# Kernel tuning notes

Hardware: AMD Instinct MI355X
Metric: run time of the kernel (lower is better)

## Reference

```python
import jax, jax.numpy as jnp
import numpy as np

N_NODES = 100000
N_EDGES = 1600000
D_FEAT = 128
HIDDEN = 128
HEADS = 4
OUT_C = HIDDEN // HEADS  # 32
N_CLASSES = 10
N_GRAPHS = 64
NEG_SLOPE = 0.2


def glorot(key, shape, fan_in, fan_out):
    s = jnp.sqrt(6.0 / (fan_in + fan_out))
    return jax.random.uniform(key, shape, minval=-s, maxval=s, dtype=jnp.float32)


def setup_inputs() -> dict:
    key = jax.random.key(0)
    ks = jax.random.split(key, 24)
    x = jax.random.normal(ks[0], (N_NODES, D_FEAT), dtype=jnp.float32)
    src = jax.random.randint(ks[1], (N_EDGES,), 0, N_NODES, dtype=jnp.int32)
    off = jax.random.randint(ks[2], (N_EDGES,), 1, N_NODES, dtype=jnp.int32)
    dst = ((src + off) % N_NODES).astype(jnp.int32)  # guarantees no self-loops
    edge_index = jnp.stack([src, dst], axis=0)
    batch = jnp.sort(jax.random.randint(ks[3], (N_NODES,), 0, N_GRAPHS, dtype=jnp.int32))
    inp = {"x": x, "edge_index": edge_index, "batch": batch}
    # GATConv layer params: W [in, H*C] (lin_l == lin_r), att_l/att_r [H, C], bias [H*C]
    ins = [D_FEAT, HIDDEN, HIDDEN]
    for i in range(3):
        k = 4 + 4 * i
        inp[f"W{i+1}"] = glorot(ks[k], (ins[i], HEADS * OUT_C), ins[i], HEADS * OUT_C)
        inp[f"al{i+1}"] = glorot(ks[k + 1], (HEADS, OUT_C), HEADS * OUT_C, 1)
        inp[f"ar{i+1}"] = glorot(ks[k + 2], (HEADS, OUT_C), HEADS * OUT_C, 1)
        inp[f"b{i+1}"] = jnp.zeros((HEADS * OUT_C,), jnp.float32)
    inp["lin1_w"] = glorot(ks[16], (HIDDEN, HIDDEN), HIDDEN, HIDDEN)
    inp["lin1_b"] = jnp.zeros((HIDDEN,), jnp.float32)
    inp["lin2_w"] = glorot(ks[17], (HIDDEN, N_CLASSES), HIDDEN, N_CLASSES)
    inp["lin2_b"] = jnp.zeros((N_CLASSES,), jnp.float32)
    return inp


def gat_layer(x, src, dst, W, att_l, att_r, bias):
    n = x.shape[0]
    H, C = att_l.shape
    xw = (x @ W).reshape(n, H, C)                       # Theta x
    al = jnp.einsum('nhc,hc->nh', xw, att_l)
    ar = jnp.einsum('nhc,hc->nh', xw, att_r)
    loop = jnp.arange(n, dtype=src.dtype)
    s = jnp.concatenate([src, loop])                    # add self-loops
    d = jnp.concatenate([dst, loop])
    logits = jax.nn.leaky_relu(al[s] + ar[d], NEG_SLOPE)  # [E+N, H]
    m = jax.ops.segment_max(logits, d, num_segments=n)    # segment softmax over dst
    e = jnp.exp(logits - m[d])
    z = jax.ops.segment_sum(e, d, num_segments=n)
    alpha = e / z[d]
    msg = xw[s] * alpha[:, :, None]                     # [E+N, H, C]
    out = jax.ops.segment_sum(msg, d, num_segments=n)   # scatter-add aggregate
    return out.reshape(n, H * C) + bias


def reference(x, edge_index, batch,
              W1, al1, ar1, b1, W2, al2, ar2, b2, W3, al3, ar3, b3,
              lin1_w, lin1_b, lin2_w, lin2_b):
    src, dst = edge_index[0], edge_index[1]
    h = jax.nn.relu(gat_layer(x, src, dst, W1, al1, ar1, b1))
    h = jax.nn.relu(gat_layer(h, src, dst, W2, al2, ar2, b2))
    h = jax.nn.relu(gat_layer(h, src, dst, W3, al3, ar3, b3))
    last = h
    # global mean pool over graphs in the batch
    s = jax.ops.segment_sum(h, batch, num_segments=N_GRAPHS)
    cnt = jax.ops.segment_sum(jnp.ones((h.shape[0],), h.dtype), batch, num_segments=N_GRAPHS)
    pooled = s / jnp.maximum(cnt, 1.0)[:, None]
    g = jax.nn.relu(pooled @ lin1_w + lin1_b)           # dropout inactive (eval)
    logits = g @ lin2_w + lin2_b
    return (jax.nn.log_softmax(logits, axis=-1), last)
```

## Files before the change

kernel.cpp:

```cpp
#include <hip/hip_runtime.h>
#include <math.h>


#define LRELU(x) ((x) > 0.f ? (x) : 0.2f*(x))
#define SH 8
#define TILE 4096
#define EPT 16
#define PSL 64

typedef __attribute__((ext_vector_type(8))) short s16x8;
typedef __attribute__((ext_vector_type(4))) float f32x4;

__device__ inline unsigned short f2bf(float f){
  unsigned u = __float_as_uint(f);
  u += 0x7fff + ((u >> 16) & 1);
  return (unsigned short)(u >> 16);
}

__global__ void k_init(int* __restrict__ bcnt, float* __restrict__ psum){
  int t = threadIdx.x;
  bcnt[t] = 0; bcnt[256 + t] = 0;
  for (int i = t; i < 8192; i += 256) psum[i] = 0.f;
}

template<bool BF16IN>
__device__ __forceinline__ void gemm_body(
    unsigned short* Wt, unsigned short* Xl,
    const void* __restrict__ Xv, const float* __restrict__ W,
    const float* __restrict__ attl, const float* __restrict__ attr,
    unsigned short* __restrict__ XW, float* __restrict__ AL, float* __restrict__ AR,
    int n, int bid, int gstride)
{
  int t = threadIdx.x;
  int lane = t & 63, w = t >> 6;
  int l15 = lane & 15, quad = lane >> 4;
  for (int i = 0; i < 64; i++){
    int e = i*256 + t;
    int k = e >> 7, nn = e & 127;
    Wt[nn*128 + ((((k>>3) ^ (nn&15))<<3) | (k&7))] = f2bf(W[e]);
  }
  int ntiles = (n + 63) >> 6;
  int r_ = t >> 2, seg = t & 3;
  for (int tile = bid; tile < ntiles; tile += gstride){
    int row0 = tile << 6;
    __syncthreads();
    {
      int grow = row0 + r_;
      unsigned short* dp = &Xl[r_*136 + seg*32];
      if (grow < n){
        if (BF16IN){
          const uint4* gp = (const uint4*)((const unsigned short*)Xv + (size_t)grow*128 + seg*32);
          #pragma unroll
          for (int i = 0; i < 4; i++) ((uint4*)dp)[i] = gp[i];
        } else {
          const float4* gp = (const float4*)((const float*)Xv + (size_t)grow*128 + seg*32);
          #pragma unroll
          for (int i = 0; i < 8; i++){
            float4 v = gp[i];
            ((unsigned*)dp)[i*2]   = (unsigned)f2bf(v.x) | ((unsigned)f2bf(v.y) << 16);
            ((unsigned*)dp)[i*2+1] = (unsigned)f2bf(v.z) | ((unsigned)f2bf(v.w) << 16);
          }
        }
      } else {
        #pragma unroll
        for (int i = 0; i < 4; i++) ((uint4*)dp)[i] = make_uint4(0,0,0,0);
      }
    }
    __syncthreads();
    f32x4 acc[4][2];
    #pragma unroll
    for (int rt = 0; rt < 4; rt++){ acc[rt][0] = (f32x4){0,0,0,0}; acc[rt][1] = (f32x4){0,0,0,0}; }
    #pragma unroll
    for (int ks = 0; ks < 4; ks++){
      s16x8 b0 = *(const s16x8*)&Wt[(w*32 + l15)*128      + (((ks*4+quad) ^ l15)<<3)];
      s16x8 b1 = *(const s16x8*)&Wt[(w*32 + 16 + l15)*128 + (((ks*4+quad) ^ l15)<<3)];
      #pragma unroll
      for (int rt = 0; rt < 4; rt++){
        s16x8 a = *(const s16x8*)&Xl[(rt*16 + l15)*136 + ks*32 + quad*8];
        acc[rt][0] = __builtin_amdgcn_mfma_f32_16x16x32_bf16(a, b0, acc[rt][0], 0, 0, 0);
        acc[rt][1] = __builtin_amdgcn_mfma_f32_16x16x32_bf16(a, b1, acc[rt][1], 0, 0, 0);
      }
    }
    __syncthreads();
    #pragma unroll
    for (int rt = 0; rt < 4; rt++)
      #pragma unroll
      for (int c2 = 0; c2 < 2; c2++)
        #pragma unroll
        for (int r = 0; r < 4; r++)
          Xl[(rt*16 + quad*4 + r)*136 + w*32 + c2*16 + l15] = f2bf(acc[rt][c2][r]);
    __syncthreads();
    {
      int grow = row0 + r_;
      if (grow < n){
        const unsigned short* sp = &Xl[r_*136 + seg*32];
        uint4 uu[4];
        #pragma unroll
        for (int i = 0; i < 4; i++) uu[i] = ((const uint4*)sp)[i];
        unsigned short* gx = XW + (size_t)grow*128 + seg*32;
        #pragma unroll
        for (int i = 0; i < 4; i++) ((uint4*)gx)[i] = uu[i];
        const unsigned* up = (const unsigned*)uu;
        const float4* alp = (const float4*)(attl + seg*32);
        const float4* arp = (const float4*)(attr + seg*32);
        float pl = 0.f, pr = 0.f;
        #pragma unroll
        for (int i = 0; i < 8; i++){
          unsigned ua = up[i*2], ub = up[i*2+1];
          float x0 = __uint_as_float(ua << 16);
          float x1 = __uint_as_float(ua & 0xffff0000u);
          float x2 = __uint_as_float(ub << 16);
          float x3 = __uint_as_float(ub & 0xffff0000u);
          float4 av = alp[i];
          float4 rv = arp[i];
          pl += x0*av.x + x1*av.y + x2*av.z + x3*av.w;
          pr += x0*rv.x + x1*rv.y + x2*rv.z + x3*rv.w;
        }
        AL[grow*4 + seg] = pl;
        AR[grow*4 + seg] = pr;
      }
    }
  }
}

template<bool BF16IN>
__global__ __launch_bounds__(256) void k_gemm(
    const void* __restrict__ Xv, const float* __restrict__ W,
    const float* __restrict__ attl, const float* __restrict__ attr,
    unsigned short* __restrict__ XW, float* __restrict__ AL, float* __restrict__ AR, int n)
{
  __shared__ unsigned short Wt[128*128];
  __shared__ unsigned short Xl[64*136];
  gemm_body<BF16IN>(Wt, Xl, Xv, W, attl, attr, XW, AL, AR, n, blockIdx.x, gridDim.x);
}

__global__ __launch_bounds__(256) void k_fuse1(
    const int* __restrict__ dst, int* __restrict__ bcnt, int E, int nparts,
    const float* __restrict__ X, const float* __restrict__ W,
    const float* __restrict__ attl, const float* __restrict__ attr,
    unsigned short* __restrict__ XW, float* __restrict__ AL, float* __restrict__ AR, int n)
{
  __shared__ unsigned short Wt[128*128];
  __shared__ unsigned short Xl[64*136];
  if ((int)blockIdx.x < nparts){
    int* lh = (int*)Wt;
    int t = threadIdx.x;
    for (int j = t; j < 512; j += 256) lh[j] = 0;
    __syncthreads();
    int base = blockIdx.x * TILE;
    int lim = min(base + TILE, E);
    for (int e = base + t; e < lim; e += 256)
      atomicAdd(&lh[dst[e] >> SH], 1);
    __syncthreads();
    for (int j = t; j < 512; j += 256){
      int v = lh[j];
      if (v) atomicAdd(&bcnt[j], v);
    }
    return;
  }
  gemm_body<false>(Wt, Xl, X, W, attl, attr, XW, AL, AR, n,
                   (int)blockIdx.x - nparts, (int)gridDim.x - nparts);
}

__global__ __launch_bounds__(256) void k_bscan(const int* __restrict__ bcnt,
    int* __restrict__ bstart, int* __restrict__ bfill, int NB, int E,
    const int* __restrict__ batch, int* __restrict__ gstart, int n){
  int t = threadIdx.x;
  if (blockIdx.x == 1){
    int g = t;
    if (g > 64) return;
    int lo = 0, hi = n;
    while (lo < hi){
      int mid = (lo + hi) >> 1;
      if (batch[mid] < g) lo = mid + 1; else hi = mid;
    }
    gstart[g] = lo;
    return;
  }
  __shared__ int c[512];
  __shared__ int ps[256];
  for (int j = t; j < 512; j += 256) c[j] = (j < NB) ? bcnt[j] : 0;
  __syncthreads();
  int b0 = 2*t;
  int v0 = c[b0], v1 = c[b0+1];
  int ts = v0 + v1;
  ps[t] = ts; __syncthreads();
  for (int off = 1; off < 256; off <<= 1){
    int x = (t >= off) ? ps[t-off] : 0; __syncthreads();
    ps[t] += x; __syncthreads();
  }
  int pre = ps[t] - ts;
  if (b0   < NB){ bstart[b0]   = pre;    bfill[b0]   = pre; }
  if (b0+1 < NB){ bstart[b0+1] = pre+v0; bfill[b0+1] = pre+v0; }
  if (t == 0) bstart[NB] = E;
}

__global__ __launch_bounds__(256) void k_part(const int* __restrict__ src,
    const int* __restrict__ dst, int* __restrict__ bfill,
    int2* __restrict__ tmp, int E){
  __shared__ int2 reorder[TILE];
  __shared__ int lhist[512], lscan[512], lgbase[512];
  __shared__ int ps[256];
  int t = threadIdx.x;
  int tb = blockIdx.x * TILE;
  int tilecnt = min(TILE, E - tb);
  for (int j = t; j < 512; j += 256) lhist[j] = 0;
  __syncthreads();
  int ss[EPT], dd[EPT], rk[EPT];
  #pragma unroll
  for (int i = 0; i < EPT; i++){
    int e = tb + t + i*256;
    if (e < E){
      ss[i] = src[e]; dd[i] = dst[e];
      rk[i] = atomicAdd(&lhist[dd[i] >> SH], 1);
    }
  }
  __syncthreads();
  int b0 = 2*t;
  int v0 = lhist[b0], v1 = lhist[b0+1];
  int ts = v0 + v1;
  ps[t] = ts; __syncthreads();
  for (int off = 1; off < 256; off <<= 1){
    int x = (t >= off) ? ps[t-off] : 0; __syncthreads();
    ps[t] += x; __syncthreads();
  }
  int pre = ps[t] - ts;
  int ex0 = pre, ex1 = pre + v0;
  lscan[b0] = ex0; lscan[b0+1] = ex1;
  if (v0 > 0){ int gb = atomicAdd(&bfill[b0],   v0); lgbase[b0]   = gb - ex0; }
  if (v1 > 0){ int gb = atomicAdd(&bfill[b0+1], v1); lgbase[b0+1] = gb - ex1; }
  __syncthreads();
  #pragma unroll
  for (int i = 0; i < EPT; i++){
    int e = tb + t + i*256;
    if (e < E){
      int b = dd[i] >> SH;
      reorder[lscan[b] + rk[i]] = make_int2(ss[i], dd[i]);
    }
  }
  __syncthreads();
  for (int j = t; j < tilecnt; j += 256){
    int2 p = reorder[j];
    tmp[lgbase[p.y >> SH] + j] = p;
  }
}

__global__ __launch_bounds__(256) void k_csr(const int2* __restrict__ tmp,
    const int* __restrict__ bstart, int* __restrict__ rp, int* __restrict__ col,
    int n, int E){
  __shared__ int lcnt[256];
  __shared__ int sc[256];
  int b = blockIdx.x, t = threadIdx.x;
  int node0 = b << SH;
  int ncnt = min(256, n - node0);
  int be = bstart[b], ee = bstart[b+1];
  lcnt[t] = 0;
  __syncthreads();
  for (int e = be + t; e < ee; e += 256)
    atomicAdd(&lcnt[tmp[e].y - node0], 1);
  __syncthreads();
  int v = lcnt[t];
  sc[t] = v;
  __syncthreads();
  for (int off = 1; off < 256; off <<= 1){
    int x = (t >= off) ? sc[t-off] : 0;
    __syncthreads();
    sc[t] += x;
    __syncthreads();
  }
  int start = be + sc[t] - v;
  lcnt[t] = start;
  if (t < ncnt) rp[node0 + t] = start;
  if (t == 0 && node0 + ncnt == n) rp[n] = E;
  __syncthreads();
  for (int e = be + t; e < ee; e += 256){
    int2 p = tmp[e];
    int pos = atomicAdd(&lcnt[p.y - node0], 1);
    col[pos] = p.x;
  }
}

template<bool BF16OUT>
__global__ __launch_bounds__(256) void k_attn(
    const unsigned short* __restrict__ XW, const float* __restrict__ AL, const float* __restrict__ AR,
    const int* __restrict__ rp, const int* __restrict__ col,
    const float* __restrict__ bias, void* __restrict__ OUT, int dbase, int nmax)
{
  __shared__ int   ws[4][512];
  __shared__ float arsh[4][4][4];
  int wv = threadIdx.x >> 6;
  int lane = threadIdx.x & 63;
  int r = lane & 15, g = lane >> 4, h2 = r >> 2;
  int d0 = dbase + (blockIdx.x*4 + wv)*4;
  if (d0 >= nmax) return;
  int d = d0 + g;
  bool valid = d < nmax;
  int dc = valid ? d : nmax-1;
  int rs = rp[dc];
  int re = valid ? rp[dc+1] : rs;
  float4 ard4 = ((const float4*)AR)[dc];
  if (r == 0) *(float4*)&arsh[wv][g][0] = ard4;
  float4 ald4 = ((const float4*)AL)[dc];
  float alh = h2==0?ald4.x : h2==1?ald4.y : h2==2?ald4.z : ald4.w;
  float arh = h2==0?ard4.x : h2==1?ard4.y : h2==2?ard4.z : ard4.w;
  float tse = alh + arh;
  float eself = __expf(fmaxf(tse, 0.2f*tse));
  const uint4* XW4 = (const uint4*)XW;
  float acc[8];
  {
    uint4 v = XW4[(size_t)dc*16 + r];
    acc[0] = eself * __uint_as_float(v.x << 16);
    acc[1] = eself * __uint_as_float(v.x & 0xffff0000u);
    acc[2] = eself * __uint_as_float(v.y << 16);
    acc[3] = eself * __uint_as_float(v.y & 0xffff0000u);
    acc[4] = eself * __uint_as_float(v.z << 16);
    acc[5] = eself * __uint_as_float(v.z & 0xffff0000u);
    acc[6] = eself * __uint_as_float(v.w << 16);
    acc[7] = eself * __uint_as_float(v.w & 0xffff0000u);
  }
  int ub0 = rp[d0];
  int ubE = rp[min(d0+4, nmax)];
  int reb = valid ? re : 0x7fffffff;
  int b1 = __shfl(reb, 0, 64);
  int b2 = __shfl(reb, 16, 64);
  int b3 = __shfl(reb, 32, 64);
  int* wsw = ws[wv];
  float zacc = eself;
  for (int cb = ub0; cb < ubE; cb += 64){
    int cnt = min(64, ubE - cb);
    if (lane < cnt){
      int e = cb + lane;
      int s = col[e];
      int eg = (e >= b1) + (e >= b2) + (e >= b3);
      float4 arr = *(const float4*)&arsh[wv][eg][0];
      float4 a = ((const float4*)AL)[s];
      float t0 = a.x + arr.x, t1 = a.y + arr.y, t2 = a.z + arr.z, t3 = a.w + arr.w;
      float w0 = __expf(fmaxf(t0, 0.2f*t0));
      float w1 = __expf(fmaxf(t1, 0.2f*t1));
      float w2 = __expf(fmaxf(t2, 0.2f*t2));
      float w3 = __expf(fmaxf(t3, 0.2f*t3));
      int s4 = s << 4;
      ((int4*)&wsw[lane*8])[0] = make_int4(s4, __float_as_int(w0), s4, __float_as_int(w1));
      ((int4*)&wsw[lane*8])[1] = make_int4(s4, __float_as_int(w2), s4, __float_as_int(w3));
    }
    int jlo = max(rs - cb, 0);
    int jhi = min(re - cb, cnt);
    #pragma unroll 4
    for (int j = jlo; j < jhi; ++j){
      int2 q = *(const int2*)&wsw[j*8 + h2*2];
      float w = __int_as_float(q.y);
      uint4 u = XW4[(unsigned)(q.x + r)];
      acc[0] = fmaf(w, __uint_as_float(u.x << 16), acc[0]);
      acc[1] = fmaf(w, __uint_as_float(u.x & 0xffff0000u), acc[1]);
      acc[2] = fmaf(w, __uint_as_float(u.y << 16), acc[2]);
      acc[3] = fmaf(w, __uint_as_float(u.y & 0xffff0000u), acc[3]);
      acc[4] = fmaf(w, __uint_as_float(u.z << 16), acc[4]);
      acc[5] = fmaf(w, __uint_as_float(u.z & 0xffff0000u), acc[5]);
      acc[6] = fmaf(w, __uint_as_float(u.w << 16), acc[6]);
      acc[7] = fmaf(w, __uint_as_float(u.w & 0xffff0000u), acc[7]);
      zacc += w;
    }
  }
  float rz = 1.f / zacc;
  float4 bb0 = ((const float4*)bias)[r*2];
  float4 bb1 = ((const float4*)bias)[r*2 + 1];
  float o[8];
  o[0] = fmaf(acc[0], rz, bb0.x); o[1] = fmaf(acc[1], rz, bb0.y);
  o[2] = fmaf(acc[2], rz, bb0.z); o[3] = fmaf(acc[3], rz, bb0.w);
  o[4] = fmaf(acc[4], rz, bb1.x); o[5] = fmaf(acc[5], rz, bb1.y);
  o[6] = fmaf(acc[6], rz, bb1.z); o[7] = fmaf(acc[7], rz, bb1.w);
  #pragma unroll
  for (int i = 0; i < 8; i++) o[i] = o[i] > 0.f ? o[i] : 0.f;
  if (valid){
    if (BF16OUT){
      uint4 pk;
      pk.x = (unsigned)f2bf(o[0]) | ((unsigned)f2bf(o[1]) << 16);
      pk.y = (unsigned)f2bf(o[2]) | ((unsigned)f2bf(o[3]) << 16);
      pk.z = (unsigned)f2bf(o[4]) | ((unsigned)f2bf(o[5]) << 16);
      pk.w = (unsigned)f2bf(o[6]) | ((unsigned)f2bf(o[7]) << 16);
      ((uint4*)OUT)[(size_t)d*16 + r] = pk;
    } else {
      float4 f0; f0.x = o[0]; f0.y = o[1]; f0.z = o[2]; f0.w = o[3];
      float4 f1; f1.x = o[4]; f1.y = o[5]; f1.z = o[6]; f1.w = o[7];
      ((float4*)OUT)[(size_t)d*32 + r*2]     = f0;
      ((float4*)OUT)[(size_t)d*32 + r*2 + 1] = f1;
    }
  }
}

__global__ __launch_bounds__(128) void k_pool(const float* __restrict__ H,
                                              const int* __restrict__ gstart,
                                              float* __restrict__ psum){
  int g = blockIdx.x >> 6, slice = blockIdx.x & (PSL-1), t = threadIdx.x;
  int s0 = gstart[g], s1 = gstart[g+1];
  int cntg = s1 - s0;
  int chunk = (cntg + PSL-1) / PSL;
  int lo = s0 + slice*chunk;
  int hi = min(lo + chunk, s1);
  if (lo >= hi) return;
  float sum = 0.f;
  for (int i = lo; i < hi; i++) sum += H[(size_t)i*128 + t];
  atomicAdd(&psum[g*128 + t], sum);
}

__global__ __launch_bounds__(128) void k_mlp(const float* __restrict__ psum,
                       const int* __restrict__ gstart,
                       const float* __restrict__ w1, const float* __restrict__ b1,
                       const float* __restrict__ w2, const float* __restrict__ b2,
                       float* __restrict__ out)
{
  __shared__ float p[128];
  __shared__ float gsh[128];
  __shared__ float lg[10];
  int g = blockIdx.x, t = threadIdx.x;
  float c = fmaxf((float)(gstart[g+1] - gstart[g]), 1.f);
  p[t] = psum[g*128 + t] / c;
  __syncthreads();
  float acc = b1[t];
  for (int k = 0; k < 128; k++) acc = fmaf(p[k], w1[k*128 + t], acc);
  gsh[t] = acc > 0.f ? acc : 0.f;
  __syncthreads();
  if (t < 10){
    float a = b2[t];
    for (int k = 0; k < 128; k++) a = fmaf(gsh[k], w2[k*10 + t], a);
    lg[t] = a;
  }
  __syncthreads();
  if (t < 10){
    float mx = lg[0];
    for (int c2 = 1; c2 < 10; c2++) mx = fmaxf(mx, lg[c2]);
    float se = 0.f;
    for (int c2 = 0; c2 < 10; c2++) se += __expf(lg[c2] - mx);
    out[g*10 + t] = lg[t] - mx - logf(se);
  }
}

extern "C" void kernel_launch(void* const* d_in, const int* in_sizes, int n_in,
                              void* d_out, int out_size, void* d_ws, size_t ws_size,
                              hipStream_t stream)
{
  const float* x    = (const float*)d_in[0];
  const int* eidx   = (const int*)d_in[1];
  const int* batch  = (const int*)d_in[2];
  const float* W[3]  = {(const float*)d_in[3], (const float*)d_in[7],  (const float*)d_in[11]};
  const float* al[3] = {(const float*)d_in[4], (const float*)d_in[8],  (const float*)d_in[12]};
  const float* ar[3] = {(const float*)d_in[5], (const float*)d_in[9],  (const float*)d_in[13]};
  const float* bs[3] = {(const float*)d_in[6], (const float*)d_in[10], (const float*)d_in[14]};
  const float* l1w = (const float*)d_in[15];
  const float* l1b = (const float*)d_in[16];
  const float* l2w = (const float*)d_in[17];
  const float* l2b = (const float*)d_in[18];
  int E = in_sizes[1] / 2;
  int n = in_sizes[2];
  const int* srcp = eidx;
  const int* dstp = eidx + E;
  int NB = (n + 255) >> SH;

  char* wsp = (char*)d_ws;
  auto alloc = [&](size_t bytes){ void* p = (void*)wsp; wsp += (bytes + 255) & ~(size_t)255; return p; };
  unsigned short* xw   = (unsigned short*)alloc((size_t)n*128*2);
  unsigned short* hbuf = (unsigned short*)alloc((size_t)n*128*2);
  float* ALb  = (float*)alloc((size_t)n*4*4);
  float* ARb  = (float*)alloc((size_t)n*4*4);
  int* rp     = (int*)alloc((size_t)(n+1)*4);
  int* col    = (int*)alloc((size_t)E*4);
  int2* tmp   = (int2*)alloc((size_t)E*8);
  int* bcnt   = (int*)alloc(512*4);
  int* bstart = (int*)alloc(513*4);
  int* bfill  = (int*)alloc(512*4);
  float* psum = (float*)alloc(64*128*4);
  int* gstart = (int*)alloc(65*4);

  float* outlog = (float*)d_out;
  float* h3     = (float*)d_out + 64*10;

  int nparts = (E + TILE - 1) / TILE;

  k_init<<<1, 256, 0, stream>>>(bcnt, psum);
  k_fuse1<<<nparts + 768, 256, 0, stream>>>(dstp, bcnt, E, nparts,
                                            x, W[0], al[0], ar[0], xw, ALb, ARb, n);
  k_bscan<<<2, 256, 0, stream>>>(bcnt, bstart, bfill, NB, E, batch, gstart, n);
  k_part <<<nparts, 256, 0, stream>>>(srcp, dstp, bfill, tmp, E);
  k_csr  <<<NB, 256, 0, stream>>>(tmp, bstart, rp, col, n, E);

  int half = ((n/2) + 15) & ~15;
  int ab1 = (half + 15) / 16;
  int ab2 = (n - half + 15) / 16;

  k_attn<true><<<ab1, 256, 0, stream>>>(xw, ALb, ARb, rp, col, bs[0], hbuf, 0, half);
  k_attn<true><<<ab2, 256, 0, stream>>>(xw, ALb, ARb, rp, col, bs[0], hbuf, half, n);
  k_gemm<true><<<768, 256, 0, stream>>>(hbuf, W[1], al[1], ar[1], xw, ALb, ARb, n);
  k_attn<true><<<ab1, 256, 0, stream>>>(xw, ALb, ARb, rp, col, bs[1], hbuf, 0, half);
  k_attn<true><<<ab2, 256, 0, stream>>>(xw, ALb, ARb, rp, col, bs[1], hbuf, half, n);
  k_gemm<true><<<768, 256, 0, stream>>>(hbuf, W[2], al[2], ar[2], xw, ALb, ARb, n);
  k_attn<false><<<ab1, 256, 0, stream>>>(xw, ALb, ARb, rp, col, bs[2], h3, 0, half);
  k_attn<false><<<ab2, 256, 0, stream>>>(xw, ALb, ARb, rp, col, bs[2], h3, half, n);

  k_pool<<<64*PSL, 128, 0, stream>>>(h3, gstart, psum);
  k_mlp <<<64, 128, 0, stream>>>(psum, gstart, l1w, l1b, l2w, l2b, outlog);
}
```

Baseline: 538.0 us.

## Pretranspose weights to bf16 once and read B fragments from global memory

All three weight matrices are converted to bf16 and transposed once in k_init, instead of each GEMM block re-converting the full 128x128 weight matrix into shared memory. The GEMM then loads B fragments straight from global memory, which L2 should serve, and writes output to a separate shared buffer so two per-tile barriers can be dropped. With less shared memory per block, the grid grows from 768 to 1024 blocks. The cost is B loads that now go to global/L2 instead of LDS on every tile.

```diff
diff --git a/kernel.cpp b/kernel.cpp
--- a/kernel.cpp
+++ b/kernel.cpp
@@ -17,16 +17,26 @@
   return (unsigned short)(u >> 16);
 }
 
-__global__ void k_init(int* __restrict__ bcnt, float* __restrict__ psum){
+__global__ void k_init(int* __restrict__ bcnt, float* __restrict__ psum,
+                       const float* __restrict__ W0, const float* __restrict__ W1,
+                       const float* __restrict__ W2, unsigned short* __restrict__ wt3){
   int t = threadIdx.x;
-  bcnt[t] = 0; bcnt[256 + t] = 0;
-  for (int i = t; i < 8192; i += 256) psum[i] = 0.f;
+  if (blockIdx.x == 0){
+    bcnt[t] = 0; bcnt[256 + t] = 0;
+    for (int i = t; i < 8192; i += 256) psum[i] = 0.f;
+    return;
+  }
+  int e = ((int)blockIdx.x - 1)*256 + t;
+  int layer = e >> 14, rem = e & 16383;
+  int k = rem >> 7, nn = rem & 127;
+  const float* Ws = layer == 0 ? W0 : (layer == 1 ? W1 : W2);
+  wt3[layer*16384 + nn*128 + k] = f2bf(Ws[k*128 + nn]);
 }
 
 template<bool BF16IN>
 __device__ __forceinline__ void gemm_body(
-    unsigned short* Wt, unsigned short* Xl,
-    const void* __restrict__ Xv, const float* __restrict__ W,
+    unsigned short* Xl, unsigned short* Cl,
+    const void* __restrict__ Xv, const unsigned short* __restrict__ Wtg,
     const float* __restrict__ attl, const float* __restrict__ attr,
     unsigned short* __restrict__ XW, float* __restrict__ AL, float* __restrict__ AR,
     int n, int bid, int gstride)
@@ -34,16 +44,12 @@
   int t = threadIdx.x;
   int lane = t & 63, w = t >> 6;
   int l15 = lane & 15, quad = lane >> 4;
-  for (int i = 0; i < 64; i++){
-    int e = i*256 + t;
-    int k = e >> 7, nn = e & 127;
-    Wt[nn*128 + ((((k>>3) ^ (nn&15))<<3) | (k&7))] = f2bf(W[e]);
-  }
   int ntiles = (n + 63) >> 6;
   int r_ = t >> 2, seg = t & 3;
+  const unsigned short* Bp0 = Wtg + (w*32 + l15)*128 + quad*8;
+  const unsigned short* Bp1 = Bp0 + 16*128;
   for (int tile = bid; tile < ntiles; tile += gstride){
     int row0 = tile << 6;
-    __syncthreads();
     {
       int grow = row0 + r_;
       unsigned short* dp = &Xl[r_*136 + seg*32];
@@ -72,8 +78,8 @@
     for (int rt = 0; rt < 4; rt++){ acc[rt][0] = (f32x4){0,0,0,0}; acc[rt][1] = (f32x4){0,0,0,0}; }
     #pragma unroll
     for (int ks = 0; ks < 4; ks++){
-      s16x8 b0 = *(const s16x8*)&Wt[(w*32 + l15)*128      + (((ks*4+quad) ^ l15)<<3)];
-      s16x8 b1 = *(const s16x8*)&Wt[(w*32 + 16 + l15)*128 + (((ks*4+quad) ^ l15)<<3)];
+      s16x8 b0 = *(const s16x8*)(Bp0 + ks*32);
+      s16x8 b1 = *(const s16x8*)(Bp1 + ks*32);
       #pragma unroll
       for (int rt = 0; rt < 4; rt++){
         s16x8 a = *(const s16x8*)&Xl[(rt*16 + l15)*136 + ks*32 + quad*8];
@@ -81,19 +87,18 @@
         acc[rt][1] = __builtin_amdgcn_mfma_f32_16x16x32_bf16(a, b1, acc[rt][1], 0, 0, 0);
       }
     }
-    __syncthreads();
     #pragma unroll
     for (int rt = 0; rt < 4; rt++)
       #pragma unroll
       for (int c2 = 0; c2 < 2; c2++)
         #pragma unroll
         for (int r = 0; r < 4; r++)
-          Xl[(rt*16 + quad*4 + r)*136 + w*32 + c2*16 + l15] = f2bf(acc[rt][c2][r]);
+          Cl[(rt*16 + quad*4 + r)*136 + w*32 + c2*16 + l15] = f2bf(acc[rt][c2][r]);
     __syncthreads();
     {
       int grow = row0 + r_;
       if (grow < n){
-        const unsigned short* sp = &Xl[r_*136 + seg*32];
+        const unsigned short* sp = &Cl[r_*136 + seg*32];
         uint4 uu[4];
         #pragma unroll
         for (int i = 0; i < 4; i++) uu[i] = ((const uint4*)sp)[i];
@@ -125,25 +130,25 @@
 
 template<bool BF16IN>
 __global__ __launch_bounds__(256) void k_gemm(
-    const void* __restrict__ Xv, const float* __restrict__ W,
+    const void* __restrict__ Xv, const unsigned short* __restrict__ Wtg,
     const float* __restrict__ attl, const float* __restrict__ attr,
     unsigned short* __restrict__ XW, float* __restrict__ AL, float* __restrict__ AR, int n)
 {
-  __shared__ unsigned short Wt[128*128];
   __shared__ unsigned short Xl[64*136];
-  gemm_body<BF16IN>(Wt, Xl, Xv, W, attl, attr, XW, AL, AR, n, blockIdx.x, gridDim.x);
+  __shared__ unsigned short Cl[64*136];
+  gemm_body<BF16IN>(Xl, Cl, Xv, Wtg, attl, attr, XW, AL, AR, n, blockIdx.x, gridDim.x);
 }
 
 __global__ __launch_bounds__(256) void k_fuse1(
     const int* __restrict__ dst, int* __restrict__ bcnt, int E, int nparts,
-    const float* __restrict__ X, const float* __restrict__ W,
+    const float* __restrict__ X, const unsigned short* __restrict__ Wtg,
     const float* __restrict__ attl, const float* __restrict__ attr,
     unsigned short* __restrict__ XW, float* __restrict__ AL, float* __restrict__ AR, int n)
 {
-  __shared__ unsigned short Wt[128*128];
   __shared__ unsigned short Xl[64*136];
+  __shared__ unsigned short Cl[64*136];
   if ((int)blockIdx.x < nparts){
-    int* lh = (int*)Wt;
+    int* lh = (int*)Xl;
     int t = threadIdx.x;
     for (int j = t; j < 512; j += 256) lh[j] = 0;
     __syncthreads();
@@ -158,7 +163,7 @@
     }
     return;
   }
-  gemm_body<false>(Wt, Xl, X, W, attl, attr, XW, AL, AR, n,
+  gemm_body<false>(Xl, Cl, X, Wtg, attl, attr, XW, AL, AR, n,
                    (int)blockIdx.x - nparts, (int)gridDim.x - nparts);
 }
 
@@ -470,15 +475,16 @@
   int* bfill  = (int*)alloc(512*4);
   float* psum = (float*)alloc(64*128*4);
   int* gstart = (int*)alloc(65*4);
+  unsigned short* wt3 = (unsigned short*)alloc(3*16384*2);
 
   float* outlog = (float*)d_out;
   float* h3     = (float*)d_out + 64*10;
 
   int nparts = (E + TILE - 1) / TILE;
 
-  k_init<<<1, 256, 0, stream>>>(bcnt, psum);
-  k_fuse1<<<nparts + 768, 256, 0, stream>>>(dstp, bcnt, E, nparts,
-                                            x, W[0], al[0], ar[0], xw, ALb, ARb, n);
+  k_init<<<193, 256, 0, stream>>>(bcnt, psum, W[0], W[1], W[2], wt3);
+  k_fuse1<<<nparts + 1024, 256, 0, stream>>>(dstp, bcnt, E, nparts,
+                                             x, wt3, al[0], ar[0], xw, ALb, ARb, n);
   k_bscan<<<2, 256, 0, stream>>>(bcnt, bstart, bfill, NB, E, batch, gstart, n);
   k_part <<<nparts, 256, 0, stream>>>(srcp, dstp, bfill, tmp, E);
   k_csr  <<<NB, 256, 0, stream>>>(tmp, bstart, rp, col, n, E);
@@ -489,10 +495,10 @@
 
   k_attn<true><<<ab1, 256, 0, stream>>>(xw, ALb, ARb, rp, col, bs[0], hbuf, 0, half);
   k_attn<true><<<ab2, 256, 0, stream>>>(xw, ALb, ARb, rp, col, bs[0], hbuf, half, n);
-  k_gemm<true><<<768, 256, 0, stream>>>(hbuf, W[1], al[1], ar[1], xw, ALb, ARb, n);
+  k_gemm<true><<<1024, 256, 0, stream>>>(hbuf, wt3 + 16384, al[1], ar[1], xw, ALb, ARb, n);
   k_attn<true><<<ab1, 256, 0, stream>>>(xw, ALb, ARb, rp, col, bs[1], hbuf, 0, half);
   k_attn<true><<<ab2, 256, 0, stream>>>(xw, ALb, ARb, rp, col, bs[1], hbuf, half, n);
-  k_gemm<true><<<768, 256, 0, stream>>>(hbuf, W[2], al[2], ar[2], xw, ALb, ARb, n);
+  k_gemm<true><<<1024, 256, 0, stream>>>(hbuf, wt3 + 32768, al[2], ar[2], xw, ALb, ARb, n);
   k_attn<false><<<ab1, 256, 0, stream>>>(xw, ALb, ARb, rp, col, bs[2], h3, 0, half);
   k_attn<false><<<ab2, 256, 0, stream>>>(xw, ALb, ARb, rp, col, bs[2], h3, half, n);
 
```

Result: faster. 518.5 us (-3.6%).
